# Optimization experiments

Measured on AMD Instinct MI355X. Metric: run time of the kernel, lower is better.

The kernel has to match this reference:

```python
import jax, jax.numpy as jnp
import numpy as np

MROPE_SECTION = [16, 24, 24]
HEAD_DIM = 128
NUM_HEADS = 16
NUM_KV_HEADS = 8
EPS = 1e-6


def rmsnorm(x, w, eps=EPS):
    xf = x.astype(jnp.float32)
    var = jnp.mean(xf * xf, axis=-1, keepdims=True)
    return (w * (xf * jax.lax.rsqrt(var + eps))).astype(x.dtype)


def rotate_half(x):
    d = x.shape[-1] // 2
    return jnp.concatenate([-x[..., d:], x[..., :d]], axis=-1)


def build_mrope(c):
    # c: [3, B, S, head_dim]; pick modality i%3 per section (non-interleaved path)
    sec = MROPE_SECTION * 2
    splits = np.cumsum(sec)[:-1]
    parts = jnp.split(c, splits, axis=-1)
    out = jnp.concatenate([p[i % 3] for i, p in enumerate(parts)], axis=-1)  # [B,S,hd]
    return out[:, None]  # unsqueeze dim 1 -> [B,1,S,hd]


def setup_inputs() -> dict:
    key = jax.random.key(0)
    ks = jax.random.split(key, 8)
    B, S, D = 2, 2048, 2048
    hd, H, KV = HEAD_DIM, NUM_HEADS, NUM_KV_HEADS
    hidden_states = jax.random.normal(ks[0], (B, S, D), jnp.float32)
    cos = jax.random.uniform(ks[1], (3, B, S, hd), jnp.float32, -1.0, 1.0)
    sin = jax.random.uniform(ks[2], (3, B, S, hd), jnp.float32, -1.0, 1.0)
    # additive causal mask [B,1,S,S]
    neg = jnp.full((S, S), -1e9, jnp.float32)
    causal = jnp.triu(neg, k=1)
    attention_mask = jnp.broadcast_to(causal[None, None], (B, 1, S, S))
    sc = 0.02
    Wq = jax.random.normal(ks[3], (D, H * hd), jnp.float32) * sc
    Wk = jax.random.normal(ks[4], (D, KV * hd), jnp.float32) * sc
    Wv = jax.random.normal(ks[5], (D, KV * hd), jnp.float32) * sc
    Wo = jax.random.normal(ks[6], (H * hd, D), jnp.float32) * sc
    q_norm_w = jnp.ones((hd,), jnp.float32)
    k_norm_w = jnp.ones((hd,), jnp.float32)
    return dict(hidden_states=hidden_states, cos=cos, sin=sin,
                attention_mask=attention_mask, Wq=Wq, Wk=Wk, Wv=Wv, Wo=Wo,
                q_norm_w=q_norm_w, k_norm_w=k_norm_w)


def reference(hidden_states, cos, sin, attention_mask, Wq, Wk, Wv, Wo, q_norm_w, k_norm_w):
    B, S, D = hidden_states.shape
    hd, H, KV = HEAD_DIM, NUM_HEADS, NUM_KV_HEADS
    groups = H // KV
    scaling = hd ** -0.5

    q = (hidden_states @ Wq).reshape(B, S, H, hd)
    k = (hidden_states @ Wk).reshape(B, S, KV, hd)
    v = (hidden_states @ Wv).reshape(B, S, KV, hd)

    q = rmsnorm(q, q_norm_w).transpose(0, 2, 1, 3)  # [B,H,S,hd]
    k = rmsnorm(k, k_norm_w).transpose(0, 2, 1, 3)  # [B,KV,S,hd]
    v = v.transpose(0, 2, 1, 3)                      # [B,KV,S,hd]

    c = build_mrope(cos)  # [B,1,S,hd]
    s = build_mrope(sin)
    q = q * c + rotate_half(q) * s
    k = k * c + rotate_half(k) * s

    # repeat_kv (GQA)
    k = jnp.repeat(k, groups, axis=1)  # [B,H,S,hd]
    v = jnp.repeat(v, groups, axis=1)

    scores = jnp.einsum('bhqd,bhkd->bhqk', q, k) * scaling + attention_mask
    attn = jax.nn.softmax(scores.astype(jnp.float32), axis=-1).astype(q.dtype)
    out = jnp.einsum('bhqk,bhkd->bqhd', attn, v).reshape(B, S, H * hd)
    return out @ Wo
```

## Files before the change

### kernel.cpp

```cpp
#include <hip/hip_runtime.h>
#include <hip/hip_bf16.h>

typedef unsigned short u16;
typedef __bf16 bf16x8 __attribute__((ext_vector_type(8)));
typedef float f32x4 __attribute__((ext_vector_type(4)));

#define B_ 2
#define S_ 2048
#define SCALE_LOG2E 0.12751743f

static __device__ __forceinline__ u16 f2bf(float f) {
    union { float f; unsigned int u; } v; v.f = f;
    unsigned int r = v.u + 0x7fffu + ((v.u >> 16) & 1u);
    return (u16)(r >> 16);
}
static __device__ __forceinline__ float bf2f(unsigned int u) {
    union { unsigned int u; float f; } v; v.u = u << 16;
    return v.f;
}

__device__ __forceinline__ void gload16(const u16* g, u16* l) {
    __builtin_amdgcn_global_load_lds(
        (const __attribute__((address_space(1))) u16*)g,
        (__attribute__((address_space(3))) u16*)l,
        16, 0, 0);
}

#define BAR()  asm volatile("s_barrier" ::: "memory")
#define WL0()  asm volatile("s_waitcnt lgkmcnt(0)" ::: "memory")
#define WVM4() asm volatile("s_waitcnt vmcnt(4)" ::: "memory")
#define WVM0() asm volatile("s_waitcnt vmcnt(0)" ::: "memory")

__global__ __launch_bounds__(256) void prep(
    const float* __restrict__ hs, u16* __restrict__ hsb,
    const float* __restrict__ Wq, const float* __restrict__ Wk,
    const float* __restrict__ Wv, const float* __restrict__ Wo,
    u16* __restrict__ wqkvb, u16* __restrict__ wob)
{
    __shared__ float tile[32][33];
    int z = blockIdx.x;
    if (z < 8192) {
        int i = z * 256 + threadIdx.x;
        float4 v = reinterpret_cast<const float4*>(hs)[i];
        ushort4 o;
        o.x = f2bf(v.x); o.y = f2bf(v.y); o.z = f2bf(v.z); o.w = f2bf(v.w);
        reinterpret_cast<ushort4*>(hsb)[i] = o;
        return;
    }
    z -= 8192;
    const float* src; u16* dst; int srs, ct, zz;
    if (z < 4096)      { src = Wq; dst = wqkvb;               srs = 2048; ct = 64; zz = z; }
    else if (z < 6144) { src = Wk; dst = wqkvb + 2048 * 2048; srs = 1024; ct = 32; zz = z - 4096; }
    else if (z < 8192) { src = Wv; dst = wqkvb + 3072 * 2048; srs = 1024; ct = 32; zz = z - 6144; }
    else               { src = Wo; dst = wob;                 srs = 2048; ct = 64; zz = z - 8192; }
    int c0 = (zz % ct) << 5, r0 = (zz / ct) << 5;
    int t = threadIdx.x, tx = t & 7, ty = t >> 3;
    float4 v = *(const float4*)&src[(size_t)(r0 + ty) * srs + c0 + 4 * tx];
    tile[ty][4 * tx + 0] = v.x; tile[ty][4 * tx + 1] = v.y;
    tile[ty][4 * tx + 2] = v.z; tile[ty][4 * tx + 3] = v.w;
    __syncthreads();
    ushort4 o;
    o.x = f2bf(tile[4 * tx + 0][ty]); o.y = f2bf(tile[4 * tx + 1][ty]);
    o.z = f2bf(tile[4 * tx + 2][ty]); o.w = f2bf(tile[4 * tx + 3][ty]);
    *(ushort4*)&dst[(size_t)(c0 + ty) * 2048 + r0 + 4 * tx] = o;
}

__device__ __forceinline__ void ldA2(bf16x8 (&aq)[2][2], const u16* bufp, int rbase, int quad) {
#pragma unroll
    for (int mm = 0; mm < 2; ++mm) {
        int r = rbase + mm * 16;
#pragma unroll
        for (int ks = 0; ks < 2; ++ks)
            aq[mm][ks] = *(const bf16x8*)(bufp + r * 64 + ((((ks << 2) | quad) ^ (r & 7)) << 3));
    }
}
__device__ __forceinline__ void ldB4(bf16x8 (&bq)[4][2], const u16* bufp, int rbase, int quad) {
#pragma unroll
    for (int n = 0; n < 4; ++n) {
        int r = rbase + n * 16;
#pragma unroll
        for (int ks = 0; ks < 2; ++ks)
            bq[n][ks] = *(const bf16x8*)(bufp + r * 64 + ((((ks << 2) | quad) ^ (r & 7)) << 3));
    }
}
__device__ __forceinline__ void mfma16(f32x4 (&acc)[8][4], const bf16x8 (&aq)[2][2],
                                       const bf16x8 (&bq)[4][2], int p) {
    __builtin_amdgcn_s_setprio(1);
#pragma unroll
    for (int n = 0; n < 4; ++n) {
#pragma unroll
        for (int mm = 0; mm < 2; ++mm) {
            acc[2 * p + mm][n] = __builtin_amdgcn_mfma_f32_16x16x32_bf16(aq[mm][0], bq[n][0], acc[2 * p + mm][n], 0, 0, 0);
            acc[2 * p + mm][n] = __builtin_amdgcn_mfma_f32_16x16x32_bf16(aq[mm][1], bq[n][1], acc[2 * p + mm][n], 0, 0, 0);
        }
    }
    __builtin_amdgcn_s_setprio(0);
}

__global__ __launch_bounds__(512, 2) void gemm256(
    const u16* __restrict__ A, const u16* __restrict__ Bt,
    u16* __restrict__ C, int M, int N, int K)
{
    __shared__ __align__(16) u16 As[2][16384];
    __shared__ __align__(16) u16 Bs[2][16384];

    int nbx = N >> 8;
    int bid = blockIdx.x, nwg = gridDim.x;
    int swz = (bid & 7) * (nwg >> 3) + (bid >> 3);
    int by = swz / nbx, bx = swz - by * nbx;
    int m0 = by << 8, n0 = bx << 8;

    int t = threadIdx.x;
    int wave = t >> 6, lane = t & 63;
    int quad = lane >> 4, l16 = lane & 15;
    int wr = wave >> 2, wc = wave & 3;

    int srow = wave * 8 + (lane >> 3);
    int sgr  = (lane & 7) ^ (lane >> 3);
    const u16* Ab = A  + (size_t)(m0 + srow) * K + sgr * 8;
    const u16* Bb = Bt + (size_t)(n0 + srow) * K + sgr * 8;
    size_t r64 = (size_t)64 * K;

#define STG(Ld, Gp, H, KO) do { \
    gload16((Gp) + (size_t)(2 * (H))     * r64 + (KO), &(Ld)[((H) * 128 +      wave * 8) * 64]); \
    gload16((Gp) + (size_t)(2 * (H) + 1) * r64 + (KO), &(Ld)[((H) * 128 + 64 + wave * 8) * 64]); \
} while (0)

    f32x4 acc[8][4];
#pragma unroll
    for (int i = 0; i < 8; ++i)
#pragma unroll
        for (int j = 0; j < 4; ++j) acc[i][j] = (f32x4){0.f, 0.f, 0.f, 0.f};

    STG(As[0], Ab, 0, 0); STG(As[0], Ab, 1, 0);
    STG(Bs[0], Bb, 0, 0); STG(Bs[0], Bb, 1, 0);
    STG(Bs[1], Bb, 0, 64); STG(Bs[1], Bb, 1, 64);
    WVM4(); BAR();

    int NT = K >> 6;
    int arb = wr * 128 + l16;
    int brb = wc * 64 + l16;
    for (int U = 0; U < NT; U += 2) {
        int kU = U << 6;
        bool sf = (U + 2 < NT);
        bf16x8 aq[2][2], bq[4][2];

        ldB4(bq, Bs[0], brb, quad);
        ldA2(aq, As[0], arb, quad);
        STG(As[1], Ab, 0, kU + 64);
        WL0(); BAR();
        __builtin_amdgcn_sched_barrier(0);
        mfma16(acc, aq, bq, 0);
        STG(As[1], Ab, 1, kU + 64);
        ldA2(aq, As[0], arb + 32, quad);
        if (sf) STG(Bs[0], Bb, 0, kU + 128);
        WL0(); __builtin_amdgcn_sched_barrier(0);
        mfma16(acc, aq, bq, 1);
        ldA2(aq, As[0], arb + 64, quad);
        if (sf) STG(Bs[0], Bb, 1, kU + 128);
        WL0(); __builtin_amdgcn_sched_barrier(0);
        mfma16(acc, aq, bq, 2);
        ldA2(aq, As[0], arb + 96, quad);
        WL0(); __builtin_amdgcn_sched_barrier(0);
        mfma16(acc, aq, bq, 3);
        if (sf) WVM4(); else WVM0();
        BAR();

        ldB4(bq, Bs[1], brb, quad);
        ldA2(aq, As[1], arb, quad);
        if (sf) STG(As[0], Ab, 0, kU + 128);
        WL0(); BAR();
        __builtin_amdgcn_sched_barrier(0);
        mfma16(acc, aq, bq, 0);
        if (sf) STG(As[0], Ab, 1, kU + 128);
        ldA2(aq, As[1], arb + 32, quad);
        if (sf) STG(Bs[1], Bb, 0, kU + 192);
        WL0(); __builtin_amdgcn_sched_barrier(0);
        mfma16(acc, aq, bq, 1);
        ldA2(aq, As[1], arb + 64, quad);
        if (sf) STG(Bs[1], Bb, 1, kU + 192);
        WL0(); __builtin_amdgcn_sched_barrier(0);
        mfma16(acc, aq, bq, 2);
        ldA2(aq, As[1], arb + 96, quad);
        WL0(); __builtin_amdgcn_sched_barrier(0);
        mfma16(acc, aq, bq, 3);
        if (sf) WVM4();
        BAR();
    }
#undef STG

#pragma unroll
    for (int m = 0; m < 8; ++m) {
        int rbase = m0 + wr * 128 + m * 16 + quad * 4;
#pragma unroll
        for (int n = 0; n < 4; ++n) {
            int col = n0 + wc * 64 + n * 16 + l16;
#pragma unroll
            for (int r = 0; r < 4; ++r)
                C[(size_t)(rbase + r) * N + col] = f2bf(acc[m][n][r]);
        }
    }
}

template<int BM, int BN, int OBF>
__global__ __launch_bounds__(256, 2) void gemm_tile(
    const u16* __restrict__ A, const u16* __restrict__ Bt,
    void* __restrict__ Cv, int M, int N, int K)
{
    constexpr int RM = BM / 32;
    constexpr int RN = BN / 32;
    constexpr int NGA = BM / 64;
    constexpr int NGB = BN / 64;
    __shared__ __align__(16) u16 As[2][BM * 32];
    __shared__ __align__(16) u16 Bs[2][BN * 32];
    int t = threadIdx.x;
    int wave = t >> 6, lane = t & 63;
    int quad = lane >> 4, l16 = lane & 15;
    int wm = (wave >> 1) * (BM / 2), wn = (wave & 1) * (BN / 2);
    int m0 = blockIdx.y * BM, n0 = blockIdx.x * BN;

    f32x4 acc[RM][RN];
#pragma unroll
    for (int i = 0; i < RM; ++i)
#pragma unroll
        for (int j = 0; j < RN; ++j)
            acc[i][j] = (f32x4){0.f, 0.f, 0.f, 0.f};

    int srow = wave * 16 + (lane >> 2);
    int sc8 = (lane & 3) << 3;
    const u16* Ap = A + (size_t)(m0 + srow) * K + sc8;
    const u16* Bp = Bt + (size_t)(n0 + srow) * K + sc8;
    size_t row64 = (size_t)64 * K;
    int lofs = (wave * 16) * 32;

#pragma unroll
    for (int g = 0; g < NGA; ++g) gload16(Ap + g * row64, &As[0][lofs + g * 64 * 32]);
#pragma unroll
    for (int g = 0; g < NGB; ++g) gload16(Bp + g * row64, &Bs[0][lofs + g * 64 * 32]);

    int it = 0;
    for (int k0 = 0; k0 < K; k0 += 32, ++it) {
        int buf = it & 1;
        __syncthreads();
        if (k0 + 32 < K) {
            u16* dA = &As[buf ^ 1][lofs];
            u16* dB = &Bs[buf ^ 1][lofs];
#pragma unroll
            for (int g = 0; g < NGA; ++g) gload16(Ap + g * row64 + k0 + 32, dA + g * 64 * 32);
#pragma unroll
            for (int g = 0; g < NGB; ++g) gload16(Bp + g * row64 + k0 + 32, dB + g * 64 * 32);
        }
        bf16x8 af[RM], bfr[RN];
#pragma unroll
        for (int i = 0; i < RM; ++i)
            af[i] = *(const bf16x8*)(&As[buf][(wm + i * 16 + l16) * 32 + quad * 8]);
#pragma unroll
        for (int j = 0; j < RN; ++j)
            bfr[j] = *(const bf16x8*)(&Bs[buf][(wn + j * 16 + l16) * 32 + quad * 8]);
#pragma unroll
        for (int i = 0; i < RM; ++i)
#pragma unroll
            for (int j = 0; j < RN; ++j)
                acc[i][j] = __builtin_amdgcn_mfma_f32_16x16x32_bf16(af[i], bfr[j], acc[i][j], 0, 0, 0);
    }

    if (OBF) {
        u16* C16 = (u16*)Cv;
#pragma unroll
        for (int i = 0; i < RM; ++i) {
            int rbase = m0 + wm + i * 16 + quad * 4;
#pragma unroll
            for (int j = 0; j < RN; ++j) {
                int col = n0 + wn + j * 16 + l16;
#pragma unroll
                for (int r = 0; r < 4; ++r)
                    C16[(size_t)(rbase + r) * N + col] = f2bf(acc[i][j][r]);
            }
        }
    } else {
        float* Cf = (float*)Cv;
#pragma unroll
        for (int i = 0; i < RM; ++i) {
            int rbase = m0 + wm + i * 16 + quad * 4;
#pragma unroll
            for (int j = 0; j < RN; ++j) {
                int col = n0 + wn + j * 16 + l16;
#pragma unroll
                for (int r = 0; r < 4; ++r)
                    Cf[(size_t)(rbase + r) * N + col] = acc[i][j][r];
            }
        }
    }
}

__global__ __launch_bounds__(256) void post(
    const u16* __restrict__ qkvb, const float* __restrict__ cosb,
    const float* __restrict__ sinb, const float* __restrict__ qw,
    const float* __restrict__ kw, u16* __restrict__ qout, u16* __restrict__ kout,
    u16* __restrict__ vbo)
{
    __shared__ u16 tile[32][36];
    int zb = blockIdx.x;
    if (zb < 24576) {
        int row = zb & 4095;
        int b = row >> 11, s = row & 2047;
        int wave = threadIdx.x >> 6, lane = threadIdx.x & 63;
        int hv = (zb >> 12) * 4 + wave;
        bool isq = hv < 16;
        int h = isq ? hv : hv - 16;
        const u16* src = qkvb + (size_t)row * 4096 + (isq ? h * 128 : 2048 + h * 128);
        int d0 = lane << 1;
        unsigned int xu = *(const unsigned int*)(src + d0);
        float x0 = bf2f(xu & 0xffffu), x1 = bf2f(xu >> 16);
        float ss = x0 * x0 + x1 * x1;
#pragma unroll
        for (int off = 32; off >= 1; off >>= 1) ss += __shfl_xor(ss, off);
        float rstd = rsqrtf(ss * (1.0f / 128.0f) + 1e-6f);
        const float* w = isq ? qw : kw;
        float2 wv = *(const float2*)(w + d0);
        float xn0 = x0 * rstd * wv.x;
        float xn1 = x1 * rstd * wv.y;
        float p0 = __shfl_xor(xn0, 32);
        float p1 = __shfl_xor(xn1, 32);
        float rh0 = (lane < 32) ? -p0 : p0;
        float rh1 = (lane < 32) ? -p1 : p1;
        int md = d0 < 16 ? 0 : d0 < 40 ? 1 : d0 < 64 ? 2 : d0 < 80 ? 0 : d0 < 104 ? 1 : 2;
        size_t cidx = ((size_t)md * (B_ * S_) + row) * 128 + d0;
        float2 c  = *(const float2*)(cosb + cidx);
        float2 sn = *(const float2*)(sinb + cidx);
        float fs = isq ? SCALE_LOG2E : 1.0f;
        float o0 = (xn0 * c.x + rh0 * sn.x) * fs;
        float o1 = (xn1 * c.y + rh1 * sn.y) * fs;
        size_t orow = isq ? ((size_t)(b * 16 + h) * 2048 + s) * 128
                          : ((size_t)(b * 8 + h) * 2048 + s) * 128;
        unsigned int pack = (unsigned int)f2bf(o0) | ((unsigned int)f2bf(o1) << 16);
        u16* dst = isq ? qout : kout;
        *(unsigned int*)(dst + orow + d0) = pack;
        return;
    }
    int z2 = zb - 24576;
    int bxi = z2 & 3, byi = (z2 >> 2) & 63, zz = z2 >> 8;
    const u16* s = qkvb + (size_t)(zz >> 3) * 2048 * 4096 + 3072 + (zz & 7) * 128;
    u16* d = vbo + (size_t)zz * 128 * 2048;
    int c0 = bxi << 5, r0 = byi << 5;
    int t = threadIdx.x, tx = t & 7, ty = t >> 3;
    ushort4 v = *(const ushort4*)&s[(size_t)(r0 + ty) * 4096 + c0 + 4 * tx];
    tile[ty][4 * tx + 0] = v.x; tile[ty][4 * tx + 1] = v.y;
    tile[ty][4 * tx + 2] = v.z; tile[ty][4 * tx + 3] = v.w;
    __syncthreads();
    ushort4 o;
    o.x = tile[4 * tx + 0][ty]; o.y = tile[4 * tx + 1][ty];
    o.z = tile[4 * tx + 2][ty]; o.w = tile[4 * tx + 3][ty];
    *(ushort4*)&d[(size_t)(c0 + ty) * 2048 + r0 + 4 * tx] = o;
}

__global__ __launch_bounds__(256, 2) void attention(
    const u16* __restrict__ qb, const u16* __restrict__ kb,
    const u16* __restrict__ vt, u16* __restrict__ ao)
{
    __shared__ __align__(16) u16 Ks[2][64 * 128];
    __shared__ __align__(16) u16 Vs[2][128 * 64];
    __shared__ __align__(16) __bf16 Ps[4][2][16 * 64];

    int t = threadIdx.x;
    int wave = t >> 6, lane = t & 63;
    int quad = lane >> 4, l16 = lane & 15;
    int bx = blockIdx.x;
    int hi = bx >> 8, u = bx & 255;
    int q5 = u & 31;
    int qt = hi ? q5 : 31 - q5;
    int bkv = ((u >> 5) << 1) | hi;
    int b = bkv >> 3, kvh = bkv & 7;
    int q0 = qt << 6;

    bf16x8 af_q[2][4];
#pragma unroll
    for (int hh = 0; hh < 2; ++hh) {
        const u16* qsrc = qb + ((size_t)(b * 16 + kvh * 2 + hh) * 2048 + q0 + wave * 16 + l16) * 128 + quad * 8;
#pragma unroll
        for (int ks = 0; ks < 4; ++ks)
            af_q[hh][ks] = *(const bf16x8*)(qsrc + ks * 32);
    }

    const u16* kbase = kb + (size_t)bkv * 2048 * 128;
    const u16* vbase = vt + (size_t)bkv * 128 * 2048;
    const u16* kg[4]; const u16* vg[4];
    u16* kl0[4]; u16* kl1[4]; u16* vl0[4]; u16* vl1[4];
    {
        int kc = lane & 15, vc = lane & 7;
#pragma unroll
        for (int j = 0; j < 4; ++j) {
            int kr = wave * 16 + j * 4 + (lane >> 4);
            kg[j] = kbase + (size_t)kr * 128 + ((kc ^ (kr & 15)) << 3);
            int vr = wave * 32 + j * 8 + (lane >> 3);
            vg[j] = vbase + (size_t)vr * 2048 + ((vc ^ (vr & 7)) << 3);
            kl0[j] = &Ks[0][(wave * 16 + j * 4) * 128];
            kl1[j] = &Ks[1][(wave * 16 + j * 4) * 128];
            vl0[j] = &Vs[0][(wave * 32 + j * 8) * 64];
            vl1[j] = &Vs[1][(wave * 32 + j * 8) * 64];
        }
    }

    f32x4 o_acc[2][8];
    float lsum[2][4];
#pragma unroll
    for (int hh = 0; hh < 2; ++hh) {
#pragma unroll
        for (int i = 0; i < 8; ++i) o_acc[hh][i] = (f32x4){0.f, 0.f, 0.f, 0.f};
#pragma unroll
        for (int r = 0; r < 4; ++r) lsum[hh][r] = 0.f;
    }

#pragma unroll
    for (int j = 0; j < 4; ++j) { gload16(kg[j], kl0[j]); gload16(vg[j], vl0[j]); }

    for (int kt = 0; kt <= qt; ++kt) {
        int buf = kt & 1;
        __syncthreads();
        if (kt < qt) {
            size_t ko = (size_t)(kt + 1) * 64 * 128;
            int vo = (kt + 1) * 64;
            if (buf) {
#pragma unroll
                for (int j = 0; j < 4; ++j) { gload16(kg[j] + ko, kl0[j]); gload16(vg[j] + vo, vl0[j]); }
            } else {
#pragma unroll
                for (int j = 0; j < 4; ++j) { gload16(kg[j] + ko, kl1[j]); gload16(vg[j] + vo, vl1[j]); }
            }
        }
        const u16* Kb = Ks[buf];
        const u16* Vb = Vs[buf];

        f32x4 sa[2][4];
#pragma unroll
        for (int nt = 0; nt < 4; ++nt) { sa[0][nt] = (f32x4){0.f,0.f,0.f,0.f}; sa[1][nt] = (f32x4){0.f,0.f,0.f,0.f}; }
#pragma unroll
        for (int nt = 0; nt < 4; ++nt)
#pragma unroll
            for (int ks = 0; ks < 4; ++ks) {
                bf16x8 bk = *(const bf16x8*)(&Kb[(nt * 16 + l16) * 128 + ((((ks << 2) | quad) ^ l16) << 3)]);
                sa[0][nt] = __builtin_amdgcn_mfma_f32_16x16x32_bf16(af_q[0][ks], bk, sa[0][nt], 0, 0, 0);
                sa[1][nt] = __builtin_amdgcn_mfma_f32_16x16x32_bf16(af_q[1][ks], bk, sa[1][nt], 0, 0, 0);
            }

        bool diag = (kt == qt);
#pragma unroll
        for (int hh = 0; hh < 2; ++hh)
#pragma unroll
            for (int r = 0; r < 4; ++r) {
                int row = quad * 4 + r;
                int qi = wave * 16 + row;
#pragma unroll
                for (int nt = 0; nt < 4; ++nt) {
                    float pe = __builtin_amdgcn_exp2f(sa[hh][nt][r]);
                    int col = nt * 16 + l16;
                    if (diag && col > qi) pe = 0.f;
                    lsum[hh][r] += pe;
                    Ps[wave][hh][row * 64 + (col ^ ((row & 7) << 3))] = (__bf16)pe;
                }
            }

#pragma unroll
        for (int ks = 0; ks < 2; ++ks) {
            int csw = (((ks << 2) | quad) ^ (l16 & 7)) << 3;
            bf16x8 pa0 = *(const bf16x8*)(&Ps[wave][0][l16 * 64 + csw]);
            bf16x8 pa1 = *(const bf16x8*)(&Ps[wave][1][l16 * 64 + csw]);
#pragma unroll
            for (int dt = 0; dt < 8; ++dt) {
                bf16x8 vf = *(const bf16x8*)(&Vb[(dt * 16 + l16) * 64 + csw]);
                o_acc[0][dt] = __builtin_amdgcn_mfma_f32_16x16x32_bf16(pa0, vf, o_acc[0][dt], 0, 0, 0);
                o_acc[1][dt] = __builtin_amdgcn_mfma_f32_16x16x32_bf16(pa1, vf, o_acc[1][dt], 0, 0, 0);
            }
        }
    }

#pragma unroll
    for (int hh = 0; hh < 2; ++hh) {
#pragma unroll
        for (int r = 0; r < 4; ++r)
#pragma unroll
            for (int off = 1; off < 16; off <<= 1) lsum[hh][r] += __shfl_xor(lsum[hh][r], off);
        size_t obase = (((size_t)b * 2048 + q0 + wave * 16) * 16 + (kvh * 2 + hh)) * 128;
#pragma unroll
        for (int r = 0; r < 4; ++r) {
            float inv = 1.0f / lsum[hh][r];
            int qrow = quad * 4 + r;
#pragma unroll
            for (int dt = 0; dt < 8; ++dt)
                ao[obase + (size_t)qrow * 2048 + dt * 16 + l16] = f2bf(o_acc[hh][dt][r] * inv);
        }
    }
}

extern "C" void kernel_launch(void* const* d_in, const int* in_sizes, int n_in,
                              void* d_out, int out_size, void* d_ws, size_t ws_size,
                              hipStream_t stream) {
    const float* hs   = (const float*)d_in[0];
    const float* cosb = (const float*)d_in[1];
    const float* sinb = (const float*)d_in[2];
    const float* Wq = (const float*)d_in[4];
    const float* Wk = (const float*)d_in[5];
    const float* Wv = (const float*)d_in[6];
    const float* Wo = (const float*)d_in[7];
    const float* qw = (const float*)d_in[8];
    const float* kw = (const float*)d_in[9];
    float* out = (float*)d_out;

    char* ws = (char*)d_ws;
    u16* hsb   = (u16*)(ws);
    u16* wqkvb = (u16*)(ws + 16777216);
    u16* wob   = (u16*)(ws + 33554432);
    u16* qkvb  = (u16*)(ws + 41943040);
    u16* qb    = (u16*)(ws + 75497472);
    u16* kb    = (u16*)(ws + 92274688);
    u16* vb    = (u16*)(ws + 100663296);
    u16* aob   = (u16*)(ws + 109051904);

    prep<<<20480, 256, 0, stream>>>(hs, hsb, Wq, Wk, Wv, Wo, wqkvb, wob);

    gemm256<<<256, 512, 0, stream>>>(hsb, wqkvb, qkvb, 4096, 4096, 2048);

    post<<<28672, 256, 0, stream>>>(qkvb, cosb, sinb, qw, kw, qb, kb, vb);

    attention<<<512, 256, 0, stream>>>(qb, kb, vb, aob);

    gemm_tile<128, 128, 0><<<dim3(16, 32), 256, 0, stream>>>(aob, wob, out, 4096, 2048, 2048);
}
```

Measured before the change: 347.2 us.

## Read K/V MFMA fragments directly from global memory instead of LDS staging

The attention kernel no longer stages K and V tiles through double-buffered shared memory with async global-to-LDS loads and per-iteration barriers. Each wave now loads its K and V MFMA operands straight from global memory, and the launch bound is raised to three blocks per CU now that LDS use is much smaller. The aim is to cut LDS traffic and `__syncthreads` overhead and to raise occupancy. The cost is that all four waves fetch the same K/V data redundantly through the caches, and there is no explicit prefetch to hide global load latency.

After: 498.2 us. 1.43x slower.

```diff
diff --git a/kernel.cpp b/kernel.cpp
--- a/kernel.cpp
+++ b/kernel.cpp
@@ -354,12 +354,10 @@
     *(ushort4*)&d[(size_t)(c0 + ty) * 2048 + r0 + 4 * tx] = o;
 }
 
-__global__ __launch_bounds__(256, 2) void attention(
+__global__ __launch_bounds__(256, 3) void attention(
     const u16* __restrict__ qb, const u16* __restrict__ kb,
     const u16* __restrict__ vt, u16* __restrict__ ao)
 {
-    __shared__ __align__(16) u16 Ks[2][64 * 128];
-    __shared__ __align__(16) u16 Vs[2][128 * 64];
     __shared__ __align__(16) __bf16 Ps[4][2][16 * 64];
 
     int t = threadIdx.x;
@@ -382,24 +380,8 @@
             af_q[hh][ks] = *(const bf16x8*)(qsrc + ks * 32);
     }
 
-    const u16* kbase = kb + (size_t)bkv * 2048 * 128;
-    const u16* vbase = vt + (size_t)bkv * 128 * 2048;
-    const u16* kg[4]; const u16* vg[4];
-    u16* kl0[4]; u16* kl1[4]; u16* vl0[4]; u16* vl1[4];
-    {
-        int kc = lane & 15, vc = lane & 7;
-#pragma unroll
-        for (int j = 0; j < 4; ++j) {
-            int kr = wave * 16 + j * 4 + (lane >> 4);
-            kg[j] = kbase + (size_t)kr * 128 + ((kc ^ (kr & 15)) << 3);
-            int vr = wave * 32 + j * 8 + (lane >> 3);
-            vg[j] = vbase + (size_t)vr * 2048 + ((vc ^ (vr & 7)) << 3);
-            kl0[j] = &Ks[0][(wave * 16 + j * 4) * 128];
-            kl1[j] = &Ks[1][(wave * 16 + j * 4) * 128];
-            vl0[j] = &Vs[0][(wave * 32 + j * 8) * 64];
-            vl1[j] = &Vs[1][(wave * 32 + j * 8) * 64];
-        }
-    }
+    const u16* kfr = kb + (size_t)bkv * 2048 * 128 + (size_t)l16 * 128 + quad * 8;
+    const u16* vfr = vt + (size_t)bkv * 128 * 2048 + (size_t)l16 * 2048 + quad * 8;
 
     f32x4 o_acc[2][8];
     float lsum[2][4];
@@ -411,26 +393,8 @@
         for (int r = 0; r < 4; ++r) lsum[hh][r] = 0.f;
     }
 
-#pragma unroll
-    for (int j = 0; j < 4; ++j) { gload16(kg[j], kl0[j]); gload16(vg[j], vl0[j]); }
-
     for (int kt = 0; kt <= qt; ++kt) {
-        int buf = kt & 1;
-        __syncthreads();
-        if (kt < qt) {
-            size_t ko = (size_t)(kt + 1) * 64 * 128;
-            int vo = (kt + 1) * 64;
-            if (buf) {
-#pragma unroll
-                for (int j = 0; j < 4; ++j) { gload16(kg[j] + ko, kl0[j]); gload16(vg[j] + vo, vl0[j]); }
-            } else {
-#pragma unroll
-                for (int j = 0; j < 4; ++j) { gload16(kg[j] + ko, kl1[j]); gload16(vg[j] + vo, vl1[j]); }
-            }
-        }
-        const u16* Kb = Ks[buf];
-        const u16* Vb = Vs[buf];
-
+        const u16* kp = kfr + (size_t)kt * 64 * 128;
         f32x4 sa[2][4];
 #pragma unroll
         for (int nt = 0; nt < 4; ++nt) { sa[0][nt] = (f32x4){0.f,0.f,0.f,0.f}; sa[1][nt] = (f32x4){0.f,0.f,0.f,0.f}; }
@@ -438,7 +402,7 @@
         for (int nt = 0; nt < 4; ++nt)
 #pragma unroll
             for (int ks = 0; ks < 4; ++ks) {
-                bf16x8 bk = *(const bf16x8*)(&Kb[(nt * 16 + l16) * 128 + ((((ks << 2) | quad) ^ l16) << 3)]);
+                bf16x8 bk = *(const bf16x8*)(kp + nt * 16 * 128 + ks * 32);
                 sa[0][nt] = __builtin_amdgcn_mfma_f32_16x16x32_bf16(af_q[0][ks], bk, sa[0][nt], 0, 0, 0);
                 sa[1][nt] = __builtin_amdgcn_mfma_f32_16x16x32_bf16(af_q[1][ks], bk, sa[1][nt], 0, 0, 0);
             }
@@ -460,6 +424,7 @@
                 }
             }
 
+        const u16* vp = vfr + kt * 64;
 #pragma unroll
         for (int ks = 0; ks < 2; ++ks) {
             int csw = (((ks << 2) | quad) ^ (l16 & 7)) << 3;
@@ -467,7 +432,7 @@
             bf16x8 pa1 = *(const bf16x8*)(&Ps[wave][1][l16 * 64 + csw]);
 #pragma unroll
             for (int dt = 0; dt < 8; ++dt) {
-                bf16x8 vf = *(const bf16x8*)(&Vb[(dt * 16 + l16) * 64 + csw]);
+                bf16x8 vf = *(const bf16x8*)(vp + (size_t)dt * 16 * 2048 + ks * 32);
                 o_acc[0][dt] = __builtin_amdgcn_mfma_f32_16x16x32_bf16(pa0, vf, o_acc[0][dt], 0, 0, 0);
                 o_acc[1][dt] = __builtin_amdgcn_mfma_f32_16x16x32_bf16(pa1, vf, o_acc[1][dt], 0, 0, 0);
             }
```

## Replace output projection GEMM with pipelined 256x128 swizzled LDS-staged kernel

Applied to the files above, without the earlier changes.

Replaces the simple double-buffered gemm_tile used for the output projection with a new 512-thread kernel using 256x128 tiles and 64-wide K steps. It reuses the QKV GEMM's XOR-swizzled global_load_lds staging, explicit vmcnt/lgkmcnt waits, sched barriers and MFMA priority boosts, plus a block-index swizzle for L2 locality. The goal is better MFMA utilisation and overlap of loads with compute in the final GEMM. The hand-tuned wait counts and buffer reuse carry a correctness risk, and with a 4096x2048 output the grid is only 256 blocks.

New measurement: 346.4 us. About the same (-0.3%).

```diff
diff --git a/kernel.cpp b/kernel.cpp
--- a/kernel.cpp
+++ b/kernel.cpp
@@ -29,7 +29,9 @@
 #define BAR()  asm volatile("s_barrier" ::: "memory")
 #define WL0()  asm volatile("s_waitcnt lgkmcnt(0)" ::: "memory")
 #define WVM4() asm volatile("s_waitcnt vmcnt(4)" ::: "memory")
+#define WVM2() asm volatile("s_waitcnt vmcnt(2)" ::: "memory")
 #define WVM0() asm volatile("s_waitcnt vmcnt(0)" ::: "memory")
+#define SB0()  __builtin_amdgcn_sched_barrier(0)
 
 __global__ __launch_bounds__(256) void prep(
     const float* __restrict__ hs, u16* __restrict__ hsb,
@@ -83,11 +85,33 @@
             bq[n][ks] = *(const bf16x8*)(bufp + r * 64 + ((((ks << 2) | quad) ^ (r & 7)) << 3));
     }
 }
+__device__ __forceinline__ void ldB2(bf16x8 (&bq)[2][2], const u16* bufp, int rbase, int quad) {
+#pragma unroll
+    for (int n = 0; n < 2; ++n) {
+        int r = rbase + n * 16;
+#pragma unroll
+        for (int ks = 0; ks < 2; ++ks)
+            bq[n][ks] = *(const bf16x8*)(bufp + r * 64 + ((((ks << 2) | quad) ^ (r & 7)) << 3));
+    }
+}
 __device__ __forceinline__ void mfma16(f32x4 (&acc)[8][4], const bf16x8 (&aq)[2][2],
                                        const bf16x8 (&bq)[4][2], int p) {
     __builtin_amdgcn_s_setprio(1);
 #pragma unroll
     for (int n = 0; n < 4; ++n) {
+#pragma unroll
+        for (int mm = 0; mm < 2; ++mm) {
+            acc[2 * p + mm][n] = __builtin_amdgcn_mfma_f32_16x16x32_bf16(aq[mm][0], bq[n][0], acc[2 * p + mm][n], 0, 0, 0);
+            acc[2 * p + mm][n] = __builtin_amdgcn_mfma_f32_16x16x32_bf16(aq[mm][1], bq[n][1], acc[2 * p + mm][n], 0, 0, 0);
+        }
+    }
+    __builtin_amdgcn_s_setprio(0);
+}
+__device__ __forceinline__ void mfma8(f32x4 (&acc)[8][2], const bf16x8 (&aq)[2][2],
+                                      const bf16x8 (&bq)[2][2], int p) {
+    __builtin_amdgcn_s_setprio(1);
+#pragma unroll
+    for (int n = 0; n < 2; ++n) {
 #pragma unroll
         for (int mm = 0; mm < 2; ++mm) {
             acc[2 * p + mm][n] = __builtin_amdgcn_mfma_f32_16x16x32_bf16(aq[mm][0], bq[n][0], acc[2 * p + mm][n], 0, 0, 0);
@@ -149,19 +173,19 @@
         ldA2(aq, As[0], arb, quad);
         STG(As[1], Ab, 0, kU + 64);
         WL0(); BAR();
-        __builtin_amdgcn_sched_barrier(0);
+        SB0();
         mfma16(acc, aq, bq, 0);
         STG(As[1], Ab, 1, kU + 64);
         ldA2(aq, As[0], arb + 32, quad);
         if (sf) STG(Bs[0], Bb, 0, kU + 128);
-        WL0(); __builtin_amdgcn_sched_barrier(0);
+        WL0(); SB0();
         mfma16(acc, aq, bq, 1);
         ldA2(aq, As[0], arb + 64, quad);
         if (sf) STG(Bs[0], Bb, 1, kU + 128);
-        WL0(); __builtin_amdgcn_sched_barrier(0);
+        WL0(); SB0();
         mfma16(acc, aq, bq, 2);
         ldA2(aq, As[0], arb + 96, quad);
-        WL0(); __builtin_amdgcn_sched_barrier(0);
+        WL0(); SB0();
         mfma16(acc, aq, bq, 3);
         if (sf) WVM4(); else WVM0();
         BAR();
@@ -170,24 +194,23 @@
         ldA2(aq, As[1], arb, quad);
         if (sf) STG(As[0], Ab, 0, kU + 128);
         WL0(); BAR();
-        __builtin_amdgcn_sched_barrier(0);
+        SB0();
         mfma16(acc, aq, bq, 0);
         if (sf) STG(As[0], Ab, 1, kU + 128);
         ldA2(aq, As[1], arb + 32, quad);
         if (sf) STG(Bs[1], Bb, 0, kU + 192);
-        WL0(); __builtin_amdgcn_sched_barrier(0);
+        WL0(); SB0();
         mfma16(acc, aq, bq, 1);
         ldA2(aq, As[1], arb + 64, quad);
         if (sf) STG(Bs[1], Bb, 1, kU + 192);
-        WL0(); __builtin_amdgcn_sched_barrier(0);
+        WL0(); SB0();
         mfma16(acc, aq, bq, 2);
         ldA2(aq, As[1], arb + 96, quad);
-        WL0(); __builtin_amdgcn_sched_barrier(0);
+        WL0(); SB0();
         mfma16(acc, aq, bq, 3);
         if (sf) WVM4();
         BAR();
     }
-#undef STG
 
 #pragma unroll
     for (int m = 0; m < 8; ++m) {
@@ -202,93 +225,85 @@
     }
 }
 
-template<int BM, int BN, int OBF>
-__global__ __launch_bounds__(256, 2) void gemm_tile(
+__global__ __launch_bounds__(512, 2) void gemm256n(
     const u16* __restrict__ A, const u16* __restrict__ Bt,
-    void* __restrict__ Cv, int M, int N, int K)
+    float* __restrict__ C, int M, int N, int K)
 {
-    constexpr int RM = BM / 32;
-    constexpr int RN = BN / 32;
-    constexpr int NGA = BM / 64;
-    constexpr int NGB = BN / 64;
-    __shared__ __align__(16) u16 As[2][BM * 32];
-    __shared__ __align__(16) u16 Bs[2][BN * 32];
+    __shared__ __align__(16) u16 As[2][16384];
+    __shared__ __align__(16) u16 Bs[2][8192];
+
+    int nbx = N >> 7;
+    int bid = blockIdx.x, nwg = gridDim.x;
+    int swz = (bid & 7) * (nwg >> 3) + (bid >> 3);
+    int by = swz / nbx, bx = swz - by * nbx;
+    int m0 = by << 8, n0 = bx << 7;
+
     int t = threadIdx.x;
     int wave = t >> 6, lane = t & 63;
     int quad = lane >> 4, l16 = lane & 15;
-    int wm = (wave >> 1) * (BM / 2), wn = (wave & 1) * (BN / 2);
-    int m0 = blockIdx.y * BM, n0 = blockIdx.x * BN;
-
-    f32x4 acc[RM][RN];
-#pragma unroll
-    for (int i = 0; i < RM; ++i)
-#pragma unroll
-        for (int j = 0; j < RN; ++j)
-            acc[i][j] = (f32x4){0.f, 0.f, 0.f, 0.f};
-
-    int srow = wave * 16 + (lane >> 2);
-    int sc8 = (lane & 3) << 3;
-    const u16* Ap = A + (size_t)(m0 + srow) * K + sc8;
-    const u16* Bp = Bt + (size_t)(n0 + srow) * K + sc8;
-    size_t row64 = (size_t)64 * K;
-    int lofs = (wave * 16) * 32;
-
-#pragma unroll
-    for (int g = 0; g < NGA; ++g) gload16(Ap + g * row64, &As[0][lofs + g * 64 * 32]);
-#pragma unroll
-    for (int g = 0; g < NGB; ++g) gload16(Bp + g * row64, &Bs[0][lofs + g * 64 * 32]);
-
-    int it = 0;
-    for (int k0 = 0; k0 < K; k0 += 32, ++it) {
-        int buf = it & 1;
-        __syncthreads();
-        if (k0 + 32 < K) {
-            u16* dA = &As[buf ^ 1][lofs];
-            u16* dB = &Bs[buf ^ 1][lofs];
-#pragma unroll
-            for (int g = 0; g < NGA; ++g) gload16(Ap + g * row64 + k0 + 32, dA + g * 64 * 32);
-#pragma unroll
-            for (int g = 0; g < NGB; ++g) gload16(Bp + g * row64 + k0 + 32, dB + g * 64 * 32);
-        }
-        bf16x8 af[RM], bfr[RN];
-#pragma unroll
-        for (int i = 0; i < RM; ++i)
-            af[i] = *(const bf16x8*)(&As[buf][(wm + i * 16 + l16) * 32 + quad * 8]);
-#pragma unroll
-        for (int j = 0; j < RN; ++j)
-            bfr[j] = *(const bf16x8*)(&Bs[buf][(wn + j * 16 + l16) * 32 + quad * 8]);
-#pragma unroll
-        for (int i = 0; i < RM; ++i)
-#pragma unroll
-            for (int j = 0; j < RN; ++j)
-                acc[i][j] = __builtin_amdgcn_mfma_f32_16x16x32_bf16(af[i], bfr[j], acc[i][j], 0, 0, 0);
-    }
-
-    if (OBF) {
-        u16* C16 = (u16*)Cv;
-#pragma unroll
-        for (int i = 0; i < RM; ++i) {
-            int rbase = m0 + wm + i * 16 + quad * 4;
-#pragma unroll
-            for (int j = 0; j < RN; ++j) {
-                int col = n0 + wn + j * 16 + l16;
-#pragma unroll
-                for (int r = 0; r < 4; ++r)
-                    C16[(size_t)(rbase + r) * N + col] = f2bf(acc[i][j][r]);
-            }
-        }
-    } else {
-        float* Cf = (float*)Cv;
-#pragma unroll
-        for (int i = 0; i < RM; ++i) {
-            int rbase = m0 + wm + i * 16 + quad * 4;
-#pragma unroll
-            for (int j = 0; j < RN; ++j) {
-                int col = n0 + wn + j * 16 + l16;
-#pragma unroll
-                for (int r = 0; r < 4; ++r)
-                    Cf[(size_t)(rbase + r) * N + col] = acc[i][j][r];
-            }
+    int wr = wave >> 2, wc = wave & 3;
+
+    int srow = wave * 8 + (lane >> 3);
+    int sgr  = (lane & 7) ^ (lane >> 3);
+    const u16* Ab = A  + (size_t)(m0 + srow) * K + sgr * 8;
+    const u16* Bb = Bt + (size_t)(n0 + srow) * K + sgr * 8;
+    size_t r64 = (size_t)64 * K;
+
+    f32x4 acc[8][2];
+#pragma unroll
+    for (int i = 0; i < 8; ++i)
+#pragma unroll
+        for (int j = 0; j < 2; ++j) acc[i][j] = (f32x4){0.f, 0.f, 0.f, 0.f};
+
+    STG(As[0], Ab, 0, 0); STG(As[0], Ab, 1, 0);
+    STG(Bs[0], Bb, 0, 0);
+    STG(Bs[1], Bb, 0, 64);
+    WVM2(); BAR();
+
+    int NT = K >> 6;
+    int arb = wr * 128 + l16;
+    int brb = wc * 32 + l16;
+    for (int U = 0; U < NT; ++U) {
+        int buf = U & 1;
+        int kU = U << 6;
+        bool sfA = (U + 1 < NT);
+        bool sfB = (U + 2 < NT);
+        bf16x8 aq[2][2], bq[2][2];
+        const u16* Ap = As[buf];
+        const u16* Bp = Bs[buf];
+        u16* An = As[buf ^ 1];
+
+        ldB2(bq, Bp, brb, quad);
+        ldA2(aq, Ap, arb, quad);
+        if (sfA) STG(An, Ab, 0, kU + 64);
+        WL0(); BAR();
+        SB0();
+        mfma8(acc, aq, bq, 0);
+        if (sfA) STG(An, Ab, 1, kU + 64);
+        ldA2(aq, Ap, arb + 32, quad);
+        if (sfB) STG(Bs[buf], Bb, 0, kU + 128);
+        WL0(); SB0();
+        mfma8(acc, aq, bq, 1);
+        ldA2(aq, Ap, arb + 64, quad);
+        WL0(); SB0();
+        mfma8(acc, aq, bq, 2);
+        ldA2(aq, Ap, arb + 96, quad);
+        WL0(); SB0();
+        mfma8(acc, aq, bq, 3);
+        if (sfB) WVM2(); else WVM0();
+        BAR();
+    }
+#undef STG
+
+#pragma unroll
+    for (int m = 0; m < 8; ++m) {
+        int rbase = m0 + wr * 128 + m * 16 + quad * 4;
+#pragma unroll
+        for (int n = 0; n < 2; ++n) {
+            int col = n0 + wc * 32 + n * 16 + l16;
+#pragma unroll
+            for (int r = 0; r < 4; ++r)
+                C[(size_t)(rbase + r) * N + col] = acc[m][n][r];
         }
     }
 }
@@ -524,5 +539,5 @@
 
     attention<<<512, 256, 0, stream>>>(qb, kb, vb, aob);
 
-    gemm_tile<128, 128, 0><<<dim3(16, 32), 256, 0, stream>>>(aob, wob, out, 4096, 2048, 2048);
-}
+    gemm256n<<<256, 512, 0, stream>>>(aob, wob, out, 4096, 2048, 2048);
+}
```
